# Optimization experiments

Measured on AMD Instinct MI355X. Metric: run time of the kernel, lower is better.

The kernel has to match this reference:

```python
import jax, jax.numpy as jnp
import numpy as np

N_LABELS = 24
LABEL_DIM = 256
NEG = -10000.0


def setup_inputs() -> dict:
    key = jax.random.key(0)
    k1, k2 = jax.random.split(key, 2)
    B, L, DIM = 8, 512, 1024
    features = jax.random.normal(k1, (B, L, DIM), dtype=jnp.float32)
    mask = jnp.ones((B, L), dtype=bool)
    w_ff = jax.random.normal(k2, (N_LABELS * LABEL_DIM * 2, DIM), dtype=jnp.float32) * 0.02
    b_ff = jnp.zeros((N_LABELS * LABEL_DIM * 2,), dtype=jnp.float32)
    bias = jnp.zeros((N_LABELS,), dtype=jnp.float32)
    return {"features": features, "mask": mask, "w_ff": w_ff, "b_ff": b_ff, "bias": bias}


def reference(features, mask, w_ff, b_ff, bias):
    B, L, _ = features.shape
    # ff -> relu -> split into start/end features per label
    x = jax.nn.relu(jnp.einsum('bld,od->blo', features, w_ff) + b_ff)  # [B,L,n_labels*label_dim*2]
    x = x.reshape(B, L, N_LABELS, LABEL_DIM, 2)
    start_f = x[..., 0]  # [B,L,n_labels,label_dim]
    end_f = x[..., 1]
    # biaffine pairwise span scores: [B, n_labels, start, end]
    scores = jnp.einsum('bsld,beld->blse', start_f, end_f) + bias[None, :, None, None]
    # remove_nan branch: replace inf/nan with -10000
    scores = jnp.where(jnp.isinf(scores) | jnp.isnan(scores), NEG, scores)
    # triangular + padding mask over (start, end)
    triu = jnp.triu(jnp.ones((L, L), dtype=bool))  # start <= end
    spans_mask = triu[None] & mask[:, :, None] & mask[:, None, :]  # [B,L,L]
    masked_scores = jnp.where(spans_mask[:, None, :, :], scores, NEG)
    return scores, masked_scores
```

## Files before the change

### kernel.cpp

```cpp
#include <hip/hip_runtime.h>
#include <hip/hip_bf16.h>

#define NLAB  24
#define LDIM  256
#define LSEQ  512
#define DDIM  1024
#define NOUT  12288
#define NEGV  (-10000.0f)
#define MOFF  50331648L

typedef __attribute__((ext_vector_type(8))) short short8;
typedef __attribute__((ext_vector_type(4))) float f32x4;
typedef unsigned short u16;
typedef unsigned int   u32;

typedef const __attribute__((address_space(1))) void gvoid_t;
typedef __attribute__((address_space(3))) void lvoid_t;

__device__ __forceinline__ u16 f2bf(float f) {
  u32 u = __builtin_bit_cast(u32, f);
  u32 r = u + 0x7FFFu + ((u >> 16) & 1u);
  return (u16)(r >> 16);
}

__device__ __forceinline__ void g2l16(const u16* g, u16* l) {
  __builtin_amdgcn_global_load_lds((gvoid_t*)g, (lvoid_t*)l, 16, 0, 0);
}

__global__ void cvt_bf16_kernel(const float* __restrict__ feat,
                                const float* __restrict__ wff,
                                u16* __restrict__ fA, u16* __restrict__ fB) {
  const long NA = 4194304L;
  const long NB = 12582912L;
  const long NQ = (NA + NB) / 4;
  long stride = (long)gridDim.x * blockDim.x;
  for (long i = (long)blockIdx.x * blockDim.x + threadIdx.x; i < NQ; i += stride) {
    long e = i * 4;
    const float* s; u16* d;
    if (e < NA) { s = feat + e;        d = fA + e; }
    else        { s = wff + (e - NA);  d = fB + (e - NA); }
    float4 v = *reinterpret_cast<const float4*>(s);
    ushort4 o;
    o.x = f2bf(v.x); o.y = f2bf(v.y); o.z = f2bf(v.z); o.w = f2bf(v.w);
    *reinterpret_cast<ushort4*>(d) = o;
  }
}

template<int LDK, bool PERM>
__device__ __forceinline__ void stage_tile(const u16* __restrict__ gbase, int row0,
                                           int k0, u16* lbuf, int t) {
#pragma unroll
  for (int l = 0; l < 4; ++l) {
    const int rt = l * 64 + (t >> 3);
    const int ce = ((t & 7) ^ (rt & 7)) << 3;
    int gr = rt;
    if (PERM) gr = (rt & ~31) | ((rt & 15) << 1) | ((rt >> 4) & 1);
    g2l16(gbase + (long)(row0 + gr) * LDK + k0 + ce, lbuf + (l * 512 + t) * 8);
  }
}

#define FRAG_OFF(r, ks, hi) (((r) * 64 + (ks) * 32 + (hi) * 8) ^ (((r) & 7) << 3))

__global__ __launch_bounds__(512, 2)
void ff_gemm256(const u16* __restrict__ A, const u16* __restrict__ B,
                const float* __restrict__ bff,
                u16* __restrict__ sf, u16* __restrict__ ef) {
  __shared__ __align__(16) u16 lds[2][2][16384];
  const int tid = threadIdx.x, lane = tid & 63, wv = tid >> 6;
  const int wm = wv >> 2, wn = wv & 3;
  const int lr = lane & 15, hi = lane >> 4;

  const int bid = blockIdx.x;
  const int wg  = (bid & 7) * 96 + (bid >> 3);
  const int tm  = wg & 15, tn = wg >> 4;
  const int rowA0 = tm * 256, rowB0 = tn * 256;

  f32x4 acc[8][4] = {};

  stage_tile<DDIM, false>(A, rowA0, 0, lds[0][0], tid);
  stage_tile<DDIM, true >(B, rowB0, 0, lds[0][1], tid);
  __syncthreads();

  int buf = 0;
  for (int t = 0; t < 16; ++t) {
    if (t < 15) {
      stage_tile<DDIM, false>(A, rowA0, (t + 1) * 64, lds[buf ^ 1][0], tid);
      stage_tile<DDIM, true >(B, rowB0, (t + 1) * 64, lds[buf ^ 1][1], tid);
    }
    const u16* La = lds[buf][0];
    const u16* Lb = lds[buf][1];
#pragma unroll
    for (int ks = 0; ks < 2; ++ks) {
      short8 af[8], bfr[4];
#pragma unroll
      for (int i = 0; i < 8; ++i) {
        const int r = wm * 128 + i * 16 + lr;
        af[i] = *reinterpret_cast<const short8*>(La + FRAG_OFF(r, ks, hi));
      }
#pragma unroll
      for (int j = 0; j < 4; ++j) {
        const int r = wn * 64 + j * 16 + lr;
        bfr[j] = *reinterpret_cast<const short8*>(Lb + FRAG_OFF(r, ks, hi));
      }
      __builtin_amdgcn_s_setprio(1);
#pragma unroll
      for (int i = 0; i < 8; ++i)
#pragma unroll
        for (int j = 0; j < 4; ++j)
          acc[i][j] = __builtin_amdgcn_mfma_f32_16x16x32_bf16(af[i], bfr[j], acc[i][j], 0, 0, 0);
      __builtin_amdgcn_s_setprio(0);
    }
    __syncthreads();
    buf ^= 1;
  }

#pragma unroll
  for (int j = 0; j < 4; ++j) {
    const int cblk = wn * 64 + j * 16;
    const int o = rowB0 + (cblk & ~31) + 2 * lr + ((cblk >> 4) & 1);
    const float bv = bff[o];
    const int label = o >> 9, d = (o >> 1) & 255, se = o & 1;
    u16* dst = se ? ef : sf;
#pragma unroll
    for (int i = 0; i < 8; ++i) {
#pragma unroll
      for (int r = 0; r < 4; ++r) {
        const int m = rowA0 + wm * 128 + i * 16 + hi * 4 + r;
        const int b = m >> 9, ll = m & 511;
        float v = acc[i][j][r] + bv;
        v = v > 0.f ? v : 0.f;
        dst[((long)(b * NLAB + label) * LSEQ + ll) * LDIM + d] = f2bf(v);
      }
    }
  }
}

#define RD_OFF(r, hi) ((4 * (r) + ((hi) ^ (((r) >> 1) & 3))) * 8)

__global__ __launch_bounds__(256, 4)
void biaffine128(const u16* __restrict__ sf, const u16* __restrict__ ef,
                 const float* __restrict__ bias, const int* __restrict__ mask,
                 float* __restrict__ out) {
  __shared__ __align__(16) u16 lds[2][2][4096];
  const int tid = threadIdx.x, lane = tid & 63, wv = tid >> 6;
  const int wm = wv >> 1, wn = wv & 1;
  const int lr = lane & 15, hi = lane >> 4;

  const int bid = blockIdx.x;
  const int wg  = (bid & 7) * 384 + (bid >> 3);
  const int bl  = wg >> 4, tile = wg & 15;
  const int tm  = tile >> 2, tn = tile & 3;
  const int b = bl / NLAB, label = bl - b * NLAB;
  const u16* Ab = sf + (long)bl * LSEQ * LDIM;
  const u16* Bb = ef + (long)bl * LSEQ * LDIM;
  const int rowA0 = tm * 128, rowB0 = tn * 128;

  const u16* gAa[2]; const u16* gBa[2]; int dsta[2];
#pragma unroll
  for (int L = 0; L < 2; ++L) {
    const int g = L * 256 + tid;
    const int r = g >> 2;
    const int c = (g & 3) ^ ((g >> 3) & 3);
    gAa[L] = Ab + (long)(rowA0 + r) * LDIM + c * 8;
    gBa[L] = Bb + (long)(rowB0 + r) * LDIM + c * 8;
    dsta[L] = g * 8;
  }

  int offA[4], offB[4];
#pragma unroll
  for (int i = 0; i < 4; ++i) { offA[i] = RD_OFF(wm * 64 + i * 16 + lr, hi); }
#pragma unroll
  for (int j = 0; j < 4; ++j) { offB[j] = RD_OFF(wn * 64 + j * 16 + lr, hi); }

  f32x4 acc[4][4] = {};

#pragma unroll
  for (int L = 0; L < 2; ++L) g2l16(gAa[L], &lds[0][0][dsta[L]]);
#pragma unroll
  for (int L = 0; L < 2; ++L) g2l16(gBa[L], &lds[0][1][dsta[L]]);
  __syncthreads();

#pragma unroll 1
  for (int t = 0; t < 8; ++t) {
    if (t < 7) {
      const int ko = (t + 1) * 32, nb = (t + 1) & 1;
#pragma unroll
      for (int L = 0; L < 2; ++L) g2l16(gAa[L] + ko, &lds[nb][0][dsta[L]]);
#pragma unroll
      for (int L = 0; L < 2; ++L) g2l16(gBa[L] + ko, &lds[nb][1][dsta[L]]);
    }
    const u16* La = lds[t & 1][0];
    const u16* Lb = lds[t & 1][1];
    short8 af[4], bfr[4];
#pragma unroll
    for (int i = 0; i < 4; ++i) af[i] = *reinterpret_cast<const short8*>(La + offA[i]);
#pragma unroll
    for (int j = 0; j < 4; ++j) bfr[j] = *reinterpret_cast<const short8*>(Lb + offB[j]);
    __builtin_amdgcn_s_setprio(1);
#pragma unroll
    for (int i = 0; i < 4; ++i)
#pragma unroll
      for (int j = 0; j < 4; ++j)
        acc[i][j] = __builtin_amdgcn_mfma_f32_16x16x32_bf16(af[i], bfr[j], acc[i][j], 0, 0, 0);
    __builtin_amdgcn_s_setprio(0);
    __syncthreads();
  }

  const float bv = bias[label];
  const long obase = (long)bl * LSEQ * LSEQ;
  bool me[4];
#pragma unroll
  for (int j = 0; j < 4; ++j) me[j] = (mask[b * LSEQ + rowB0 + wn * 64 + j * 16 + lr] != 0);
#pragma unroll
  for (int i = 0; i < 4; ++i) {
#pragma unroll
    for (int r = 0; r < 4; ++r) {
      const int s = rowA0 + wm * 64 + i * 16 + hi * 4 + r;
      const bool ms = (mask[b * LSEQ + s] != 0);
      const long rbase = obase + (long)s * LSEQ;
#pragma unroll
      for (int j = 0; j < 4; ++j) {
        const int e = rowB0 + wn * 64 + j * 16 + lr;
        float v = acc[i][j][r] + bv;
        u32 bits = __builtin_bit_cast(u32, v);
        if ((bits & 0x7F800000u) == 0x7F800000u) v = NEGV;
        out[rbase + e] = v;
        const bool keep = (s <= e) && ms && me[j];
        out[MOFF + rbase + e] = keep ? v : NEGV;
      }
    }
  }
}

extern "C" void kernel_launch(void* const* d_in, const int* in_sizes, int n_in,
                              void* d_out, int out_size, void* d_ws, size_t ws_size,
                              hipStream_t stream) {
  const float* feat = (const float*)d_in[0];
  const int*   mask = (const int*)d_in[1];
  const float* wff  = (const float*)d_in[2];
  const float* bff  = (const float*)d_in[3];
  const float* bias = (const float*)d_in[4];
  float* out = (float*)d_out;

  u16* fA = (u16*)d_ws;
  u16* fB = fA + 4194304L;
  u16* sf = fB + 12582912L;
  u16* ef = sf + 25165824L;

  cvt_bf16_kernel<<<2048, 256, 0, stream>>>(feat, wff, fA, fB);
  ff_gemm256<<<768, 512, 0, stream>>>(fA, fB, bff, sf, ef);
  biaffine128<<<3072, 256, 0, stream>>>(sf, ef, bias, mask, out);
}
```

Before: 258.9 us.

## Enlarge biaffine tiles to 256x256 with two sequential 128-column phases

The biaffine kernel moves from 128x128 tiles on 256-thread blocks to 256x256 tiles on 512-thread blocks. Each block covers its 256 end columns in two phases of 128, so every phase uses 8x2 MFMA accumulators per wave. This cuts the launch to 768 blocks. The A tile is reloaded from global in each phase rather than kept resident, so the gain in operand reuse is partial and comes at the cost of fewer blocks and a serialized epilogue per phase.

```diff
diff --git a/kernel.cpp b/kernel.cpp
--- a/kernel.cpp
+++ b/kernel.cpp
@@ -137,96 +137,107 @@
 
 #define RD_OFF(r, hi) ((4 * (r) + ((hi) ^ (((r) >> 1) & 3))) * 8)
 
-__global__ __launch_bounds__(256, 4)
-void biaffine128(const u16* __restrict__ sf, const u16* __restrict__ ef,
-                 const float* __restrict__ bias, const int* __restrict__ mask,
-                 float* __restrict__ out) {
-  __shared__ __align__(16) u16 lds[2][2][4096];
+__global__ __launch_bounds__(512, 4)
+void biaffine256s(const u16* __restrict__ sf, const u16* __restrict__ ef,
+                  const float* __restrict__ bias, const int* __restrict__ mask,
+                  float* __restrict__ out) {
+  __shared__ __align__(16) u16 lds[2][12288];
   const int tid = threadIdx.x, lane = tid & 63, wv = tid >> 6;
-  const int wm = wv >> 1, wn = wv & 1;
+  const int wm = wv >> 2, wn = wv & 3;
   const int lr = lane & 15, hi = lane >> 4;
 
   const int bid = blockIdx.x;
-  const int wg  = (bid & 7) * 384 + (bid >> 3);
-  const int bl  = wg >> 4, tile = wg & 15;
-  const int tm  = tile >> 2, tn = tile & 3;
+  const int wg  = (bid & 7) * 96 + (bid >> 3);
+  const int bl  = wg >> 2, tile = wg & 3;
+  const int tm  = tile >> 1, tn = tile & 1;
   const int b = bl / NLAB, label = bl - b * NLAB;
   const u16* Ab = sf + (long)bl * LSEQ * LDIM;
   const u16* Bb = ef + (long)bl * LSEQ * LDIM;
-  const int rowA0 = tm * 128, rowB0 = tn * 128;
-
-  const u16* gAa[2]; const u16* gBa[2]; int dsta[2];
+  const int rowA0 = tm * 256, rowB0 = tn * 256;
+
+  const u16* gAa[2]; int dstA[2];
 #pragma unroll
   for (int L = 0; L < 2; ++L) {
-    const int g = L * 256 + tid;
+    const int g = L * 512 + tid;
     const int r = g >> 2;
     const int c = (g & 3) ^ ((g >> 3) & 3);
     gAa[L] = Ab + (long)(rowA0 + r) * LDIM + c * 8;
-    gBa[L] = Bb + (long)(rowB0 + r) * LDIM + c * 8;
-    dsta[L] = g * 8;
-  }
-
-  int offA[4], offB[4];
-#pragma unroll
-  for (int i = 0; i < 4; ++i) { offA[i] = RD_OFF(wm * 64 + i * 16 + lr, hi); }
-#pragma unroll
-  for (int j = 0; j < 4; ++j) { offB[j] = RD_OFF(wn * 64 + j * 16 + lr, hi); }
-
-  f32x4 acc[4][4] = {};
-
-#pragma unroll
-  for (int L = 0; L < 2; ++L) g2l16(gAa[L], &lds[0][0][dsta[L]]);
-#pragma unroll
-  for (int L = 0; L < 2; ++L) g2l16(gBa[L], &lds[0][1][dsta[L]]);
-  __syncthreads();
-
-#pragma unroll 1
-  for (int t = 0; t < 8; ++t) {
-    if (t < 7) {
-      const int ko = (t + 1) * 32, nb = (t + 1) & 1;
-#pragma unroll
-      for (int L = 0; L < 2; ++L) g2l16(gAa[L] + ko, &lds[nb][0][dsta[L]]);
-#pragma unroll
-      for (int L = 0; L < 2; ++L) g2l16(gBa[L] + ko, &lds[nb][1][dsta[L]]);
-    }
-    const u16* La = lds[t & 1][0];
-    const u16* Lb = lds[t & 1][1];
-    short8 af[4], bfr[4];
-#pragma unroll
-    for (int i = 0; i < 4; ++i) af[i] = *reinterpret_cast<const short8*>(La + offA[i]);
-#pragma unroll
-    for (int j = 0; j < 4; ++j) bfr[j] = *reinterpret_cast<const short8*>(Lb + offB[j]);
-    __builtin_amdgcn_s_setprio(1);
-#pragma unroll
-    for (int i = 0; i < 4; ++i)
-#pragma unroll
-      for (int j = 0; j < 4; ++j)
-        acc[i][j] = __builtin_amdgcn_mfma_f32_16x16x32_bf16(af[i], bfr[j], acc[i][j], 0, 0, 0);
-    __builtin_amdgcn_s_setprio(0);
-    __syncthreads();
-  }
+    dstA[L] = g * 8;
+  }
+  const int rb = tid >> 2;
+  const int cb = (tid & 3) ^ ((tid >> 3) & 3);
+  const u16* gB0 = Bb + (long)(rowB0 + rb) * LDIM + cb * 8;
+  const int dstB = 8192 + tid * 8;
+
+  int offA[8], offB[2];
+#pragma unroll
+  for (int i = 0; i < 8; ++i) offA[i] = RD_OFF(wm * 128 + i * 16 + lr, hi);
+#pragma unroll
+  for (int j = 0; j < 2; ++j) offB[j] = 8192 + RD_OFF(wn * 32 + j * 16 + lr, hi);
 
   const float bv = bias[label];
   const long obase = (long)bl * LSEQ * LSEQ;
-  bool me[4];
-#pragma unroll
-  for (int j = 0; j < 4; ++j) me[j] = (mask[b * LSEQ + rowB0 + wn * 64 + j * 16 + lr] != 0);
-#pragma unroll
-  for (int i = 0; i < 4; ++i) {
-#pragma unroll
-    for (int r = 0; r < 4; ++r) {
-      const int s = rowA0 + wm * 64 + i * 16 + hi * 4 + r;
-      const bool ms = (mask[b * LSEQ + s] != 0);
-      const long rbase = obase + (long)s * LSEQ;
-#pragma unroll
-      for (int j = 0; j < 4; ++j) {
-        const int e = rowB0 + wn * 64 + j * 16 + lr;
-        float v = acc[i][j][r] + bv;
-        u32 bits = __builtin_bit_cast(u32, v);
-        if ((bits & 0x7F800000u) == 0x7F800000u) v = NEGV;
-        out[rbase + e] = v;
-        const bool keep = (s <= e) && ms && me[j];
-        out[MOFF + rbase + e] = keep ? v : NEGV;
+
+#pragma unroll 1
+  for (int ph = 0; ph < 2; ++ph) {
+    const u16* gBp = gB0 + (long)ph * 128 * LDIM;
+    const int ebase = rowB0 + ph * 128;
+
+    f32x4 acc[8][2] = {};
+
+#pragma unroll
+    for (int L = 0; L < 2; ++L) g2l16(gAa[L], &lds[0][dstA[L]]);
+    g2l16(gBp, &lds[0][dstB]);
+    __syncthreads();
+
+#pragma unroll 1
+    for (int t = 0; t < 8; ++t) {
+      if (t < 7) {
+        const int ko = (t + 1) * 32, nb = (t + 1) & 1;
+#pragma unroll
+        for (int L = 0; L < 2; ++L) g2l16(gAa[L] + ko, &lds[nb][dstA[L]]);
+        g2l16(gBp + ko, &lds[nb][dstB]);
+      }
+      const u16* Lc = lds[t & 1];
+      short8 bfr[2];
+#pragma unroll
+      for (int j = 0; j < 2; ++j) bfr[j] = *reinterpret_cast<const short8*>(Lc + offB[j]);
+      __builtin_amdgcn_s_setprio(1);
+#pragma unroll
+      for (int ihalf = 0; ihalf < 2; ++ihalf) {
+        short8 a4[4];
+#pragma unroll
+        for (int i = 0; i < 4; ++i) a4[i] = *reinterpret_cast<const short8*>(Lc + offA[ihalf * 4 + i]);
+#pragma unroll
+        for (int i = 0; i < 4; ++i)
+#pragma unroll
+          for (int j = 0; j < 2; ++j)
+            acc[ihalf * 4 + i][j] = __builtin_amdgcn_mfma_f32_16x16x32_bf16(a4[i], bfr[j], acc[ihalf * 4 + i][j], 0, 0, 0);
+      }
+      __builtin_amdgcn_s_setprio(0);
+      __syncthreads();
+    }
+
+    bool me[2];
+#pragma unroll
+    for (int j = 0; j < 2; ++j) me[j] = (mask[b * LSEQ + ebase + wn * 32 + j * 16 + lr] != 0);
+#pragma unroll
+    for (int i = 0; i < 8; ++i) {
+#pragma unroll
+      for (int r = 0; r < 4; ++r) {
+        const int s = rowA0 + wm * 128 + i * 16 + hi * 4 + r;
+        const bool ms = (mask[b * LSEQ + s] != 0);
+        const long rbase = obase + (long)s * LSEQ;
+#pragma unroll
+        for (int j = 0; j < 2; ++j) {
+          const int e = ebase + wn * 32 + j * 16 + lr;
+          float v = acc[i][j][r] + bv;
+          u32 bits = __builtin_bit_cast(u32, v);
+          if ((bits & 0x7F800000u) == 0x7F800000u) v = NEGV;
+          out[rbase + e] = v;
+          const bool keep = (s <= e) && ms && me[j];
+          out[MOFF + rbase + e] = keep ? v : NEGV;
+        }
       }
     }
   }
@@ -249,5 +260,5 @@
 
   cvt_bf16_kernel<<<2048, 256, 0, stream>>>(feat, wff, fA, fB);
   ff_gemm256<<<768, 512, 0, stream>>>(fA, fB, bff, sf, ef);
-  biaffine128<<<3072, 256, 0, stream>>>(sf, ef, bias, mask, out);
-}
+  biaffine256s<<<768, 512, 0, stream>>>(sf, ef, bias, mask, out);
+}
```

New measurement: 380.0 us. 1.47x slower.

## Load full K panel into LDS once in biaffine kernel, drop per-step barriers

Applied to the files above, without the earlier changes.

The biaffine kernel now stages the entire 128x256 A and B tiles (128 KB of LDS) in one burst instead of double-buffering 32-wide K slices over eight steps. It then runs all eight MFMA k-steps with no __syncthreads between them and uses a 32-way XOR swizzle for the wider rows. This removes the per-iteration barriers and the load/compute handoff, but the large LDS footprint cuts occupancy to about one block per CU and exposes the full load latency before any compute starts.

```diff
diff --git a/kernel.cpp b/kernel.cpp
--- a/kernel.cpp
+++ b/kernel.cpp
@@ -135,13 +135,11 @@
   }
 }
 
-#define RD_OFF(r, hi) ((4 * (r) + ((hi) ^ (((r) >> 1) & 3))) * 8)
-
-__global__ __launch_bounds__(256, 4)
-void biaffine128(const u16* __restrict__ sf, const u16* __restrict__ ef,
-                 const float* __restrict__ bias, const int* __restrict__ mask,
-                 float* __restrict__ out) {
-  __shared__ __align__(16) u16 lds[2][2][4096];
+__global__ __launch_bounds__(256)
+void biaffine128f(const u16* __restrict__ sf, const u16* __restrict__ ef,
+                  const float* __restrict__ bias, const int* __restrict__ mask,
+                  float* __restrict__ out) {
+  __shared__ __align__(16) u16 lds[65536];
   const int tid = threadIdx.x, lane = tid & 63, wv = tid >> 6;
   const int wm = wv >> 1, wn = wv & 1;
   const int lr = lane & 15, hi = lane >> 4;
@@ -151,51 +149,43 @@
   const int bl  = wg >> 4, tile = wg & 15;
   const int tm  = tile >> 2, tn = tile & 3;
   const int b = bl / NLAB, label = bl - b * NLAB;
-  const u16* Ab = sf + (long)bl * LSEQ * LDIM;
-  const u16* Bb = ef + (long)bl * LSEQ * LDIM;
-  const int rowA0 = tm * 128, rowB0 = tn * 128;
-
-  const u16* gAa[2]; const u16* gBa[2]; int dsta[2];
-#pragma unroll
-  for (int L = 0; L < 2; ++L) {
-    const int g = L * 256 + tid;
-    const int r = g >> 2;
-    const int c = (g & 3) ^ ((g >> 3) & 3);
-    gAa[L] = Ab + (long)(rowA0 + r) * LDIM + c * 8;
-    gBa[L] = Bb + (long)(rowB0 + r) * LDIM + c * 8;
-    dsta[L] = g * 8;
-  }
-
-  int offA[4], offB[4];
-#pragma unroll
-  for (int i = 0; i < 4; ++i) { offA[i] = RD_OFF(wm * 64 + i * 16 + lr, hi); }
-#pragma unroll
-  for (int j = 0; j < 4; ++j) { offB[j] = RD_OFF(wn * 64 + j * 16 + lr, hi); }
+  const u16* Ab = sf + ((long)bl * LSEQ + tm * 128) * LDIM;
+  const u16* Bb = ef + ((long)bl * LSEQ + tn * 128) * LDIM;
+
+  {
+    const int r0 = tid >> 5, c0 = tid & 31;
+#pragma unroll
+    for (int L = 0; L < 16; ++L) {
+      const int row = r0 + 8 * L;
+      const int cg  = c0 ^ (row & 31);
+      const long go = (long)row * LDIM + cg * 8;
+      const int  dd = (row * 32 + c0) * 8;
+      g2l16(Ab + go, &lds[dd]);
+      g2l16(Bb + go, &lds[32768 + dd]);
+    }
+  }
+  __syncthreads();
+
+  int rA[4], rB[4];
+#pragma unroll
+  for (int i = 0; i < 4; ++i) rA[i] = wm * 64 + i * 16 + lr;
+#pragma unroll
+  for (int j = 0; j < 4; ++j) rB[j] = wn * 64 + j * 16 + lr;
 
   f32x4 acc[4][4] = {};
-
-#pragma unroll
-  for (int L = 0; L < 2; ++L) g2l16(gAa[L], &lds[0][0][dsta[L]]);
-#pragma unroll
-  for (int L = 0; L < 2; ++L) g2l16(gBa[L], &lds[0][1][dsta[L]]);
-  __syncthreads();
-
-#pragma unroll 1
-  for (int t = 0; t < 8; ++t) {
-    if (t < 7) {
-      const int ko = (t + 1) * 32, nb = (t + 1) & 1;
-#pragma unroll
-      for (int L = 0; L < 2; ++L) g2l16(gAa[L] + ko, &lds[nb][0][dsta[L]]);
-#pragma unroll
-      for (int L = 0; L < 2; ++L) g2l16(gBa[L] + ko, &lds[nb][1][dsta[L]]);
-    }
-    const u16* La = lds[t & 1][0];
-    const u16* Lb = lds[t & 1][1];
+#pragma unroll
+  for (int ks = 0; ks < 8; ++ks) {
     short8 af[4], bfr[4];
 #pragma unroll
-    for (int i = 0; i < 4; ++i) af[i] = *reinterpret_cast<const short8*>(La + offA[i]);
-#pragma unroll
-    for (int j = 0; j < 4; ++j) bfr[j] = *reinterpret_cast<const short8*>(Lb + offB[j]);
+    for (int i = 0; i < 4; ++i) {
+      const int off = rA[i] * 256 + (((ks * 4 + hi) ^ (rA[i] & 31)) << 3);
+      af[i] = *reinterpret_cast<const short8*>(&lds[off]);
+    }
+#pragma unroll
+    for (int j = 0; j < 4; ++j) {
+      const int off = rB[j] * 256 + (((ks * 4 + hi) ^ (rB[j] & 31)) << 3);
+      bfr[j] = *reinterpret_cast<const short8*>(&lds[32768 + off]);
+    }
     __builtin_amdgcn_s_setprio(1);
 #pragma unroll
     for (int i = 0; i < 4; ++i)
@@ -203,11 +193,11 @@
       for (int j = 0; j < 4; ++j)
         acc[i][j] = __builtin_amdgcn_mfma_f32_16x16x32_bf16(af[i], bfr[j], acc[i][j], 0, 0, 0);
     __builtin_amdgcn_s_setprio(0);
-    __syncthreads();
   }
 
   const float bv = bias[label];
   const long obase = (long)bl * LSEQ * LSEQ;
+  const int rowA0 = tm * 128, rowB0 = tn * 128;
   bool me[4];
 #pragma unroll
   for (int j = 0; j < 4; ++j) me[j] = (mask[b * LSEQ + rowB0 + wn * 64 + j * 16 + lr] != 0);
@@ -249,5 +239,5 @@
 
   cvt_bf16_kernel<<<2048, 256, 0, stream>>>(feat, wff, fA, fB);
   ff_gemm256<<<768, 512, 0, stream>>>(fA, fB, bff, sf, ef);
-  biaffine128<<<3072, 256, 0, stream>>>(sf, ef, bias, mask, out);
-}
+  biaffine128f<<<3072, 256, 0, stream>>>(sf, ef, bias, mask, out);
+}
```

Result: no change. 258.7 us (-0.1%).
